# Kernel tuning notes

Measured on AMD Instinct MI355X. Metric: run time of the kernel, lower is better.

The kernel has to match this reference:

```python
import jax, jax.numpy as jnp
import numpy as np

B, D, S = 16, 512, 1500   # batch, input_size, seq_len
E, K, L = 8, 1024, 8      # embedding_size, num_embeddings, num_layers
TAU = 1.0
EPS = 1e-12               # F.normalize default eps


def setup_inputs() -> dict:
    key = jax.random.key(0)
    ks = jax.random.split(key, 5)
    x = jax.random.normal(ks[0], (B, D, S), dtype=jnp.float32)
    # weight-norm parametrized 1x1 conv params (v direction, g magnitude, bias)
    in_v = jax.random.normal(ks[1], (L, E, D), dtype=jnp.float32) * 0.05
    in_g = jnp.ones((L, E), dtype=jnp.float32)
    in_b = jnp.zeros((L, E), dtype=jnp.float32)
    out_v = jax.random.normal(ks[2], (L, D, E), dtype=jnp.float32) * 0.05
    out_g = jnp.ones((L, D), dtype=jnp.float32)
    out_b = jnp.zeros((L, D), dtype=jnp.float32)
    codebook = jax.random.normal(ks[3], (L, K, E), dtype=jnp.float32)
    return dict(x=x, in_v=in_v, in_g=in_g, in_b=in_b,
                out_v=out_v, out_g=out_g, out_b=out_b, codebook=codebook)


def _wn(v, g):
    # torch weight_norm (dim=0): w = g * v / ||v|| with norm over all dims except out-channel
    n = jnp.sqrt(jnp.sum(v * v, axis=1, keepdims=True))
    return g[:, None] * v / n


def _l2norm(x):
    # F.normalize(p=2, eps=1e-12)
    n = jnp.linalg.norm(x, axis=-1, keepdims=True)
    return x / jnp.maximum(n, EPS)


def _vq_layer(xr, iv, ig, ib, ov, og, ob, cb):
    Wi = _wn(iv, ig)                                              # [E, D]
    x_proj = jnp.einsum('ed,bds->bes', Wi, xr) + ib[:, None]      # [B, E, S]
    xf = x_proj.transpose(0, 2, 1).reshape(B * S, E)              # [B*S, E]
    xn = _l2norm(xf)
    cn = _l2norm(cb)                                              # [K, E]
    dist = (jnp.sum(xn * xn, axis=1, keepdims=True)
            - 2.0 * (xn @ cn.T)
            + jnp.sum(cn * cn, axis=1)[None, :])                  # [B*S, K]
    logits = -dist / TAU
    idxs = jnp.argmax(-dist, axis=1).reshape(B, S)                # [B, S]
    xq = cb[idxs].transpose(0, 2, 1)                              # [B, E, S] (un-normalized codebook)
    commit = jnp.mean((x_proj - jax.lax.stop_gradient(xq)) ** 2, axis=(1, 2))  # per-batch
    cbloss = jnp.mean((xq - jax.lax.stop_gradient(x_proj)) ** 2, axis=(1, 2))
    xq_st = x_proj + jax.lax.stop_gradient(xq - x_proj)           # straight-through
    Wo = _wn(ov, og)                                              # [D, E]
    xq_out = jnp.einsum('de,bes->bds', Wo, xq_st) + ob[:, None]   # [B, D, S]
    return xq_out, logits, idxs, commit, cbloss


def reference(x, in_v, in_g, in_b, out_v, out_g, out_b, codebook):
    # eval mode: all layers active, mask all-ones => masked mean == plain batch mean
    xq_sum = jnp.zeros_like(x)
    xr = x
    idxs_l, logits_l = [], []
    commit = jnp.float32(0.0)
    cbl = jnp.float32(0.0)
    for i in range(L):
        xq, lg, ix, cl, bl = _vq_layer(xr, in_v[i], in_g[i], in_b[i],
                                       out_v[i], out_g[i], out_b[i], codebook[i])
        xq_sum = xq_sum + xq
        xr = xr - xq
        commit = commit + jnp.mean(cl)
        cbl = cbl + jnp.mean(bl)
        idxs_l.append(ix)
        logits_l.append(lg)
    x_idxs = jnp.stack(idxs_l, axis=1)     # [B, L, S]
    x_logits = jnp.stack(logits_l, axis=1) # [B*S, L, K]
    return xq_sum, x_idxs, x_logits, commit, cbl
```

## Files before the change

kernel.cpp:

```cpp
#include <hip/hip_runtime.h>

constexpr int Lx = 8;
constexpr int Bx = 16;
constexpr int Dx = 512;
constexpr int Sx = 1500;
constexpr int Ex = 8;
constexpr int Kx = 1024;
constexpr int BS = Bx * Sx;
#define EPSF 1e-12f

__device__ __forceinline__ void lds_barrier() {
    asm volatile("s_waitcnt lgkmcnt(0)" ::: "memory");
    __builtin_amdgcn_s_barrier();
    asm volatile("" ::: "memory");
}

__device__ __forceinline__ void gload_lds16(const void* g, void* l) {
    __builtin_amdgcn_global_load_lds(
        (const __attribute__((address_space(1))) void*)g,
        (__attribute__((address_space(3))) void*)l, 16, 0, 0);
}

__global__ __launch_bounds__(64) void k_wn_in(const float* __restrict__ v,
                                              const float* __restrict__ g,
                                              float* __restrict__ WiT) {
    int row = blockIdx.x;
    int l = row >> 3, e = row & 7;
    int lane = threadIdx.x;
    const float* vr = v + row * Dx;
    float s = 0.f;
    for (int j = lane; j < Dx; j += 64) { float t = vr[j]; s += t * t; }
    for (int off = 32; off; off >>= 1) s += __shfl_down(s, off);
    s = __shfl(s, 0);
    float scale = g[row] / sqrtf(s);
    for (int j = lane; j < Dx; j += 64)
        WiT[((size_t)l * Dx + j) * Ex + e] = vr[j] * scale;
}

__global__ __launch_bounds__(256) void k_wn_out_cb(const float* __restrict__ ov,
                                                   const float* __restrict__ og,
                                                   const float* __restrict__ cb,
                                                   float* __restrict__ Wo,
                                                   float* __restrict__ cn,
                                                   float* __restrict__ cc,
                                                   double* __restrict__ acc) {
    int r = blockIdx.x * blockDim.x + threadIdx.x;
    if (r == 0) *acc = 0.0;
    if (r < Lx * Dx) {
        const float* vr = ov + r * Ex;
        float s = 0.f;
        #pragma unroll
        for (int e = 0; e < Ex; e++) s += vr[e] * vr[e];
        float sc = og[r] / sqrtf(s);
        #pragma unroll
        for (int e = 0; e < Ex; e++) Wo[r * Ex + e] = vr[e] * sc;
    } else {
        int q = r - Lx * Dx;
        if (q < Lx * Kx) {
            const float* vr = cb + q * Ex;
            float s = 0.f;
            #pragma unroll
            for (int e = 0; e < Ex; e++) s += vr[e] * vr[e];
            float n = fmaxf(sqrtf(s), EPSF);
            float s2 = 0.f, qv[Ex];
            #pragma unroll
            for (int e = 0; e < Ex; e++) { qv[e] = vr[e] / n; s2 += qv[e] * qv[e]; }
            #pragma unroll
            for (int e = 0; e < Ex; e++) cn[q * Ex + e] = qv[e];
            cc[q] = s2;
        }
    }
}

__global__ __launch_bounds__(256, 4) void k_mega(const float* __restrict__ x,
                                                 const float* __restrict__ WiT,
                                                 const float* __restrict__ ibias,
                                                 const float* __restrict__ Wo,
                                                 const float* __restrict__ obias,
                                                 const float* __restrict__ cb,
                                                 const float* __restrict__ cn,
                                                 const float* __restrict__ cc,
                                                 float* __restrict__ out0,
                                                 float* __restrict__ oidx,
                                                 float* __restrict__ logits,
                                                 double* __restrict__ acc) {
    __shared__ float4 cnA[Kx];
    __shared__ float4 cnB[Kx];
    __shared__ float  ccs[Kx];
    __shared__ float  xprojs[Ex * 32];
    __shared__ float  xqs[Ex * 32];
    __shared__ float  bred[4];
    float* red = (float*)cnA;

    const int t = threadIdx.x;
    const int col = t & 31;
    const int g = t >> 5;
    const int wave = t >> 6, lane = t & 63;
    const int c = blockIdx.x * 32 + col;
    const int b = c / Sx;
    const int s = c - b * Sx;
    const float* xcol = x + (size_t)b * Dx * Sx + s;

    float xr[64];
    #pragma unroll
    for (int i = 0; i < 64; i++) xr[i] = xcol[(size_t)(g * 64 + i) * Sx];

    float lossp = 0.f;

    for (int l = 0; l < Lx; l++) {
        const float4* wt = (const float4*)(WiT + (size_t)l * Dx * Ex);
        float pacc[8] = {0, 0, 0, 0, 0, 0, 0, 0};
        #pragma unroll
        for (int i = 0; i < 64; i++) {
            int d = g * 64 + i;
            float4 w0 = wt[d * 2 + 0];
            float4 w1 = wt[d * 2 + 1];
            float v = xr[i];
            pacc[0] += w0.x * v; pacc[1] += w0.y * v;
            pacc[2] += w0.z * v; pacc[3] += w0.w * v;
            pacc[4] += w1.x * v; pacc[5] += w1.y * v;
            pacc[6] += w1.z * v; pacc[7] += w1.w * v;
        }
        #pragma unroll
        for (int e = 0; e < 8; e++) red[(g * 8 + e) * 32 + col] = pacc[e];
        lds_barrier();

        {
            float sum = 0.f;
            #pragma unroll
            for (int gg = 0; gg < 8; gg++) sum += red[(gg * 8 + g) * 32 + col];
            xprojs[g * 32 + col] = sum + ibias[l * Ex + g];
        }
        lds_barrier();

        {
            const char* cs = (const char*)(cn + (size_t)l * Kx * Ex);
            const char* zs = (const char*)(cc + (size_t)l * Kx);
            #pragma unroll
            for (int q = 0; q < 4; q++) {
                const char* srcp = cs + (size_t)(wave * 256 + q * 64 + lane) * 32;
                gload_lds16(srcp,      (char*)cnA + wave * 4096 + q * 1024);
                gload_lds16(srcp + 16, (char*)cnB + wave * 4096 + q * 1024);
            }
            gload_lds16(zs + (size_t)(wave * 64 + lane) * 16, (char*)ccs + wave * 1024);
            asm volatile("s_waitcnt vmcnt(0)" ::: "memory");
        }
        lds_barrier();

        for (int pass = 0; pass < 2; pass++) {
            const int colbase = wave * 8 + pass * 4;
            float xn2[4][8];
            float xc[4], best[4];
            int bk[4];
            float* lrow[4];
            #pragma unroll
            for (int c4 = 0; c4 < 4; c4++) {
                int mycol = colbase + c4;
                int mc = blockIdx.x * 32 + mycol;
                float xp[8]; float xx2 = 0.f;
                #pragma unroll
                for (int e = 0; e < 8; e++) {
                    xp[e] = xprojs[e * 32 + mycol];
                    xx2 += xp[e] * xp[e];
                }
                float nrm = fmaxf(sqrtf(xx2), EPSF);
                float xx = 0.f;
                #pragma unroll
                for (int e = 0; e < 8; e++) {
                    float xnv = xp[e] / nrm;
                    xx += xnv * xnv;
                    xn2[c4][e] = 2.f * xnv;
                }
                xc[c4] = xx;
                best[c4] = -3.0e38f;
                bk[c4] = 0;
                lrow[c4] = logits + ((size_t)mc * Lx + l) * Kx;
            }
            #pragma unroll 2
            for (int j = 0; j < 16; j++) {
                int k = j * 64 + lane;
                float4 a  = cnA[k];
                float4 b4 = cnB[k];
                float  cv = ccs[k];
                #pragma unroll
                for (int c4 = 0; c4 < 4; c4++) {
                    float dot2 = xn2[c4][0] * a.x  + xn2[c4][1] * a.y +
                                 xn2[c4][2] * a.z  + xn2[c4][3] * a.w +
                                 xn2[c4][4] * b4.x + xn2[c4][5] * b4.y +
                                 xn2[c4][6] * b4.z + xn2[c4][7] * b4.w;
                    float lg = -(xc[c4] - dot2 + cv);
                    lrow[c4][k] = lg;
                    if (lg > best[c4]) { best[c4] = lg; bk[c4] = k; }
                }
            }
            #pragma unroll
            for (int c4 = 0; c4 < 4; c4++) {
                float bv = best[c4]; int bi = bk[c4];
                for (int off = 32; off; off >>= 1) {
                    float ov = __shfl_xor(bv, off);
                    int   oi = __shfl_xor(bi, off);
                    if (ov > bv || (ov == bv && oi < bi)) { bv = ov; bi = oi; }
                }
                int mycol = colbase + c4;
                int mc = blockIdx.x * 32 + mycol;
                int mb = mc / Sx, ms = mc - mb * Sx;
                if (lane == 0) oidx[((size_t)mb * Lx + l) * Sx + ms] = (float)bi;
                if (lane < 8) {
                    float q = cb[((size_t)l * Kx + bi) * Ex + lane];
                    xqs[lane * 32 + mycol] = q;
                    float dl = xprojs[lane * 32 + mycol] - q;
                    lossp += dl * dl;
                }
            }
        }
        lds_barrier();

        float xq[8];
        #pragma unroll
        for (int e = 0; e < 8; e++) xq[e] = xqs[e * 32 + col];
        const float4* wo4 = (const float4*)(Wo + (size_t)l * Dx * Ex);
        const float* obl = obias + l * Dx;
        #pragma unroll
        for (int i = 0; i < 64; i++) {
            int d = g * 64 + i;
            float4 w0 = wo4[d * 2 + 0];
            float4 w1 = wo4[d * 2 + 1];
            float dsum = w0.x * xq[0] + w0.y * xq[1] + w0.z * xq[2] + w0.w * xq[3] +
                         w1.x * xq[4] + w1.y * xq[5] + w1.z * xq[6] + w1.w * xq[7] +
                         obl[d];
            xr[i] -= dsum;
        }
    }

    float* ocol = out0 + (size_t)b * Dx * Sx + s;
    #pragma unroll
    for (int i = 0; i < 64; i++) {
        float xv = xcol[(size_t)(g * 64 + i) * Sx];
        ocol[(size_t)(g * 64 + i) * Sx] = xv - xr[i];
    }

    for (int off = 32; off; off >>= 1) lossp += __shfl_down(lossp, off);
    if (lane == 0) bred[wave] = lossp;
    lds_barrier();
    if (t == 0)
        atomicAdd(acc, (double)(bred[0] + bred[1] + bred[2] + bred[3]));
}

__global__ void k_scalar(const double* __restrict__ acc,
                         float* __restrict__ commit, float* __restrict__ cbl) {
    if (threadIdx.x == 0) {
        float v = (float)(*acc / (double)((size_t)Bx * Ex * Sx));
        *commit = v;
        *cbl = v;
    }
}

extern "C" void kernel_launch(void* const* d_in, const int* in_sizes, int n_in,
                              void* d_out, int out_size, void* d_ws, size_t ws_size,
                              hipStream_t stream) {
    const float* x     = (const float*)d_in[0];
    const float* in_v  = (const float*)d_in[1];
    const float* in_g  = (const float*)d_in[2];
    const float* in_b  = (const float*)d_in[3];
    const float* out_v = (const float*)d_in[4];
    const float* out_g = (const float*)d_in[5];
    const float* out_b = (const float*)d_in[6];
    const float* cb    = (const float*)d_in[7];

    float* out = (float*)d_out;
    float* out0     = out;
    float* oidx     = out + 12288000;
    float* ologits  = out + 12480000;
    float* ocommit  = out + 209088000;
    float* ocbl     = out + 209088001;

    char* w = (char*)d_ws;
    float*  WiT   = (float*)(w);
    float*  Wo    = (float*)(w + 131072);
    float*  cn    = (float*)(w + 262144);
    float*  cc    = (float*)(w + 524288);
    double* acc   = (double*)(w + 557056);

    k_wn_in<<<Lx * Ex, 64, 0, stream>>>(in_v, in_g, WiT);
    k_wn_out_cb<<<(Lx * Dx + Lx * Kx) / 256, 256, 0, stream>>>(out_v, out_g, cb,
                                                               Wo, cn, cc, acc);
    k_mega<<<BS / 32, 256, 0, stream>>>(x, WiT, in_b, Wo, out_b, cb, cn, cc,
                                        out0, oidx, ologits, acc);
    k_scalar<<<1, 64, 0, stream>>>(acc, ocommit, ocbl);
}
```

Before: 732.1 us.

## Double block threads to 512 and prefetch codebook into registers early

Each block now runs 512 threads, so every thread holds 32 instead of 64 residual values and each wave scores 4 columns in a single pass instead of two. The direct global-to-LDS codebook loads are replaced by register loads issued at the start of each layer, then written to shared memory after the projection. This is meant to raise parallelism per column tile, cut register pressure, and hide the codebook fetch latency behind the projection. The cost is more barrier traffic, a 16-way reduction in the projection, and possibly lower occupancy with launch bounds (512,4).

```diff
diff --git a/kernel.cpp b/kernel.cpp
--- a/kernel.cpp
+++ b/kernel.cpp
@@ -13,12 +13,6 @@
     asm volatile("s_waitcnt lgkmcnt(0)" ::: "memory");
     __builtin_amdgcn_s_barrier();
     asm volatile("" ::: "memory");
-}
-
-__device__ __forceinline__ void gload_lds16(const void* g, void* l) {
-    __builtin_amdgcn_global_load_lds(
-        (const __attribute__((address_space(1))) void*)g,
-        (__attribute__((address_space(3))) void*)l, 16, 0, 0);
 }
 
 __global__ __launch_bounds__(64) void k_wn_in(const float* __restrict__ v,
@@ -72,7 +66,7 @@
     }
 }
 
-__global__ __launch_bounds__(256, 4) void k_mega(const float* __restrict__ x,
+__global__ __launch_bounds__(512, 4) void k_mega(const float* __restrict__ x,
                                                  const float* __restrict__ WiT,
                                                  const float* __restrict__ ibias,
                                                  const float* __restrict__ Wo,
@@ -89,7 +83,7 @@
     __shared__ float  ccs[Kx];
     __shared__ float  xprojs[Ex * 32];
     __shared__ float  xqs[Ex * 32];
-    __shared__ float  bred[4];
+    __shared__ float  bred[8];
     float* red = (float*)cnA;
 
     const int t = threadIdx.x;
@@ -101,18 +95,24 @@
     const int s = c - b * Sx;
     const float* xcol = x + (size_t)b * Dx * Sx + s;
 
-    float xr[64];
+    float xr[32];
     #pragma unroll
-    for (int i = 0; i < 64; i++) xr[i] = xcol[(size_t)(g * 64 + i) * Sx];
+    for (int i = 0; i < 32; i++) xr[i] = xcol[(size_t)(g * 32 + i) * Sx];
 
     float lossp = 0.f;
 
     for (int l = 0; l < Lx; l++) {
+        const float4* cn4 = (const float4*)(cn + (size_t)l * Kx * Ex);
+        const float2* cc2 = (const float2*)(cc + (size_t)l * Kx);
+        float4 ra0 = cn4[t * 2],           rb0 = cn4[t * 2 + 1];
+        float4 ra1 = cn4[(t + 512) * 2],   rb1 = cn4[(t + 512) * 2 + 1];
+        float2 rcc = cc2[t];
+
         const float4* wt = (const float4*)(WiT + (size_t)l * Dx * Ex);
         float pacc[8] = {0, 0, 0, 0, 0, 0, 0, 0};
         #pragma unroll
-        for (int i = 0; i < 64; i++) {
-            int d = g * 64 + i;
+        for (int i = 0; i < 32; i++) {
+            int d = g * 32 + i;
             float4 w0 = wt[d * 2 + 0];
             float4 w1 = wt[d * 2 + 1];
             float v = xr[i];
@@ -125,37 +125,27 @@
         for (int e = 0; e < 8; e++) red[(g * 8 + e) * 32 + col] = pacc[e];
         lds_barrier();
 
+        if (t < 256) {
+            float sum = 0.f;
+            #pragma unroll
+            for (int gg = 0; gg < 16; gg++) sum += red[(gg * 8 + g) * 32 + col];
+            xprojs[g * 32 + col] = sum + ibias[l * Ex + g];
+        }
+        lds_barrier();
+
+        cnA[t] = ra0; cnA[t + 512] = ra1;
+        cnB[t] = rb0; cnB[t + 512] = rb1;
+        ((float2*)ccs)[t] = rcc;
+        lds_barrier();
+
         {
-            float sum = 0.f;
-            #pragma unroll
-            for (int gg = 0; gg < 8; gg++) sum += red[(gg * 8 + g) * 32 + col];
-            xprojs[g * 32 + col] = sum + ibias[l * Ex + g];
-        }
-        lds_barrier();
-
-        {
-            const char* cs = (const char*)(cn + (size_t)l * Kx * Ex);
-            const char* zs = (const char*)(cc + (size_t)l * Kx);
-            #pragma unroll
-            for (int q = 0; q < 4; q++) {
-                const char* srcp = cs + (size_t)(wave * 256 + q * 64 + lane) * 32;
-                gload_lds16(srcp,      (char*)cnA + wave * 4096 + q * 1024);
-                gload_lds16(srcp + 16, (char*)cnB + wave * 4096 + q * 1024);
-            }
-            gload_lds16(zs + (size_t)(wave * 64 + lane) * 16, (char*)ccs + wave * 1024);
-            asm volatile("s_waitcnt vmcnt(0)" ::: "memory");
-        }
-        lds_barrier();
-
-        for (int pass = 0; pass < 2; pass++) {
-            const int colbase = wave * 8 + pass * 4;
             float xn2[4][8];
             float xc[4], best[4];
             int bk[4];
             float* lrow[4];
             #pragma unroll
             for (int c4 = 0; c4 < 4; c4++) {
-                int mycol = colbase + c4;
+                int mycol = wave * 4 + c4;
                 int mc = blockIdx.x * 32 + mycol;
                 float xp[8]; float xx2 = 0.f;
                 #pragma unroll
@@ -201,7 +191,7 @@
                     int   oi = __shfl_xor(bi, off);
                     if (ov > bv || (ov == bv && oi < bi)) { bv = ov; bi = oi; }
                 }
-                int mycol = colbase + c4;
+                int mycol = wave * 4 + c4;
                 int mc = blockIdx.x * 32 + mycol;
                 int mb = mc / Sx, ms = mc - mb * Sx;
                 if (lane == 0) oidx[((size_t)mb * Lx + l) * Sx + ms] = (float)bi;
@@ -221,8 +211,8 @@
         const float4* wo4 = (const float4*)(Wo + (size_t)l * Dx * Ex);
         const float* obl = obias + l * Dx;
         #pragma unroll
-        for (int i = 0; i < 64; i++) {
-            int d = g * 64 + i;
+        for (int i = 0; i < 32; i++) {
+            int d = g * 32 + i;
             float4 w0 = wo4[d * 2 + 0];
             float4 w1 = wo4[d * 2 + 1];
             float dsum = w0.x * xq[0] + w0.y * xq[1] + w0.z * xq[2] + w0.w * xq[3] +
@@ -234,16 +224,20 @@
 
     float* ocol = out0 + (size_t)b * Dx * Sx + s;
     #pragma unroll
-    for (int i = 0; i < 64; i++) {
-        float xv = xcol[(size_t)(g * 64 + i) * Sx];
-        ocol[(size_t)(g * 64 + i) * Sx] = xv - xr[i];
+    for (int i = 0; i < 32; i++) {
+        float xv = xcol[(size_t)(g * 32 + i) * Sx];
+        ocol[(size_t)(g * 32 + i) * Sx] = xv - xr[i];
     }
 
     for (int off = 32; off; off >>= 1) lossp += __shfl_down(lossp, off);
     if (lane == 0) bred[wave] = lossp;
-    lds_barrier();
-    if (t == 0)
-        atomicAdd(acc, (double)(bred[0] + bred[1] + bred[2] + bred[3]));
+    __syncthreads();
+    if (t == 0) {
+        float tot = 0.f;
+        #pragma unroll
+        for (int wv = 0; wv < 8; wv++) tot += bred[wv];
+        atomicAdd(acc, (double)tot);
+    }
 }
 
 __global__ void k_scalar(const double* __restrict__ acc,
@@ -284,7 +278,7 @@
     k_wn_in<<<Lx * Ex, 64, 0, stream>>>(in_v, in_g, WiT);
     k_wn_out_cb<<<(Lx * Dx + Lx * Kx) / 256, 256, 0, stream>>>(out_v, out_g, cb,
                                                                Wo, cn, cc, acc);
-    k_mega<<<BS / 32, 256, 0, stream>>>(x, WiT, in_b, Wo, out_b, cb, cn, cc,
+    k_mega<<<BS / 32, 512, 0, stream>>>(x, WiT, in_b, Wo, out_b, cb, cn, cc,
                                         out0, oidx, ologits, acc);
     k_scalar<<<1, 64, 0, stream>>>(acc, ocommit, ocbl);
 }
```

Result: faster. 700.3 us (-4.3%).
